# Performance work log

Measured on AMD Instinct MI355X. Metric: run time of the kernel, lower is better.

## Reference

```python
import jax, jax.numpy as jnp
import numpy as np
import math

B, N, D, H, F = 2, 2048, 512, 8, 2048
DH = D // H
LN_EPS = 1e-5
PHASE_ALPHA = 0.1


def _layernorm(x, g, b):
    mu = jnp.mean(x, axis=-1, keepdims=True)
    var = jnp.mean(jnp.square(x - mu), axis=-1, keepdims=True)
    return (x - mu) * jax.lax.rsqrt(var + LN_EPS) * g + b


def setup_inputs() -> dict:
    key = jax.random.key(0)
    ks = jax.random.split(key, 16)
    s = 0.02
    return {
        "h": jax.random.normal(ks[0], (B, N, D), dtype=jnp.float32),
        "phases": jax.random.normal(ks[1], (B, N, H), dtype=jnp.float32),
        "mask": jnp.zeros((B, N), dtype=bool),
        "Wq": jax.random.normal(ks[2], (D, D), dtype=jnp.float32) * s,
        "Wk": jax.random.normal(ks[3], (D, D), dtype=jnp.float32) * s,
        "Wp": jax.random.normal(ks[4], (D, H), dtype=jnp.float32) * s,
        "bp": jnp.zeros((H,), dtype=jnp.float32),
        "Wv": jax.random.normal(ks[5], (D, D), dtype=jnp.float32) * s,
        "Wo": jax.random.normal(ks[6], (D, D), dtype=jnp.float32) * s,
        "W1": jax.random.normal(ks[7], (D, F), dtype=jnp.float32) * s,
        "b1": jnp.zeros((F,), dtype=jnp.float32),
        "W2": jax.random.normal(ks[8], (F, D), dtype=jnp.float32) * s,
        "b2": jnp.zeros((D,), dtype=jnp.float32),
        "g1": jnp.ones((D,), dtype=jnp.float32),
        "be1": jnp.zeros((D,), dtype=jnp.float32),
        "g2": jnp.ones((D,), dtype=jnp.float32),
        "be2": jnp.zeros((D,), dtype=jnp.float32),
        "Wph": jax.random.normal(ks[9], (D, H), dtype=jnp.float32) * s,
        "bph": jnp.zeros((H,), dtype=jnp.float32),
    }


def reference(h, phases, mask, Wq, Wk, Wp, bp, Wv, Wo, W1, b1, W2, b2, g1, be1, g2, be2, Wph, bph):
    # --- HarmonicEdgeLayer ---
    Q = (h @ Wq).reshape(B, N, H, DH)  # (B,N,H,dh)
    K = (h @ Wk).reshape(B, N, H, DH)
    scores = jnp.einsum("bnhd,bmhd->bhnm", Q, K) / math.sqrt(DH)  # (B,H,N,N)
    ph = h @ Wp + bp                       # (B,N,H)
    phi = jnp.transpose(ph, (0, 2, 1))     # (B,H,N)
    harmonic = jnp.cos(phi[:, :, :, None] - phi[:, :, None, :])  # (B,H,N,N)
    scores = scores * (1.0 + harmonic) * 0.5
    scores = jnp.where(mask[:, None, None, :], -jnp.inf, scores)
    edge_weights = jax.nn.softmax(scores, axis=-1)  # (B,H,N,N)

    # --- HarmonicNodeUpdate ---
    V = (h @ Wv).reshape(B, N, H, DH)
    messages = jnp.einsum("bhnm,bmhd->bnhd", edge_weights, V).reshape(B, N, D)
    messages = messages @ Wo
    h1 = _layernorm(h + messages, g1, be1)
    ffn = jax.nn.gelu(h1 @ W1 + b1, approximate=False) @ W2 + b2
    h2 = _layernorm(h1 + ffn, g2, be2)

    # --- PhaseUpdate ---
    phases_new = phases + PHASE_ALPHA * jnp.tanh(h2 @ Wph + bph) * math.pi

    # convergence metric
    delta = jnp.mean(jnp.linalg.norm(h2 - h, axis=-1))
    return h2, phases_new, delta
```

## Files before the change

### kernel.cpp

```cpp
#include <hip/hip_runtime.h>
#include <math.h>

#define BB 2
#define NN 2048
#define DD 512
#define HH 8
#define DHH 64
#define FF 2048
#define MROWS (BB*NN)
#define LN_EPS 1e-5f
#define PHASE_ALPHA 0.1f
#define PI_F 3.14159265358979323846f
#define SCALE 0.125f
#define QLD (3*DD)

typedef __attribute__((ext_vector_type(8))) short  bf16x8;
typedef __attribute__((ext_vector_type(4))) float  f32x4;
typedef __attribute__((ext_vector_type(4))) unsigned short us4;

__device__ __forceinline__ unsigned short f2bf(float x) {
    unsigned int u = __float_as_uint(x);
    u += 0x7fffu + ((u >> 16) & 1u);
    return (unsigned short)(u >> 16);
}

__global__ __launch_bounds__(256) void convert_bf16_kernel(
    const float* __restrict__ X, unsigned short* __restrict__ Y, int n8)
{
    int i = blockIdx.x*256 + threadIdx.x;
    if (i >= n8) return;
    const float4 a = *(const float4*)&X[i*8];
    const float4 b = *(const float4*)&X[i*8 + 4];
    uint4 o;
    o.x = (unsigned)f2bf(a.x) | ((unsigned)f2bf(a.y) << 16);
    o.y = (unsigned)f2bf(a.z) | ((unsigned)f2bf(a.w) << 16);
    o.z = (unsigned)f2bf(b.x) | ((unsigned)f2bf(b.y) << 16);
    o.w = (unsigned)f2bf(b.z) | ((unsigned)f2bf(b.w) << 16);
    *(uint4*)&Y[i*8] = o;
}

__global__ __launch_bounds__(256) void wtrans_kernel(
    const float* __restrict__ W, unsigned short* __restrict__ WT, int K, int N)
{
    __shared__ unsigned short T[32][33];
    const int k0 = blockIdx.y*32, n0 = blockIdx.x*32;
    const int r = threadIdx.x >> 3, cc = (threadIdx.x & 7)*4;
    float4 v = *(const float4*)&W[(size_t)(k0 + r)*N + n0 + cc];
    T[cc+0][r] = f2bf(v.x); T[cc+1][r] = f2bf(v.y);
    T[cc+2][r] = f2bf(v.z); T[cc+3][r] = f2bf(v.w);
    __syncthreads();
    us4 o; o.x = T[r][cc]; o.y = T[r][cc+1]; o.z = T[r][cc+2]; o.w = T[r][cc+3];
    *(us4*)&WT[(size_t)(n0 + r)*K + k0 + cc] = o;
}

__global__ __launch_bounds__(256) void vtrans_kernel(
    const unsigned short* __restrict__ qkv, unsigned short* __restrict__ VT)
{
    __shared__ unsigned short T[32][33];
    const int b = blockIdx.z;
    const int n0 = blockIdx.x*32, c0 = blockIdx.y*32;
    const int r = threadIdx.x >> 3, cc = (threadIdx.x & 7)*4;
    us4 v = *(const us4*)&qkv[((size_t)b*NN + n0 + r)*QLD + 2*DD + c0 + cc];
    T[cc+0][r] = v.x; T[cc+1][r] = v.y; T[cc+2][r] = v.z; T[cc+3][r] = v.w;
    __syncthreads();
    const int cg = c0 + r;
    const int hh = cg >> 6, dh = cg & 63;
    us4 o; o.x = T[r][cc]; o.y = T[r][cc+1]; o.z = T[r][cc+2]; o.w = T[r][cc+3];
    *(us4*)&VT[(((size_t)b*HH + hh)*DHH + dh)*NN + n0 + cc] = o;
}

template<int BM, int BN, int SPLITK, int OUTBF16, int BIAS, int ACT, int ATOMIC>
__global__ __launch_bounds__(256, 2) void mfma_gemm(
    const unsigned short* __restrict__ A, const unsigned short* __restrict__ BT,
    const float* __restrict__ bias, void* __restrict__ Cout,
    int M, int Nc, int K)
{
    constexpr int FM = BM/32, FN = BN/32;
    constexpr int ROWS = BM + BN;
    constexpr int NLOAD = ROWS*8/256;
    __shared__ unsigned short Ss[ROWS][72];

    const int tid = threadIdx.x;
    const int w = tid >> 6, lane = tid & 63;
    const int c = lane & 15, g = lane >> 4;
    const int wr = w >> 1, wc = w & 1;
    const int bm = blockIdx.y*BM, bn = blockIdx.x*BN;
    const int k0 = (SPLITK > 1) ? blockIdx.z * (K / SPLITK) : 0;
    const int NT = (K / SPLITK) / 64;

    f32x4 zero = {0.f, 0.f, 0.f, 0.f};
    f32x4 acc[FM][FN];
    #pragma unroll
    for (int i = 0; i < FM; ++i)
        #pragma unroll
        for (int j = 0; j < FN; ++j) acc[i][j] = zero;

    uint4 pf[NLOAD];
    #pragma unroll
    for (int l = 0; l < NLOAD; ++l) {
        const int i = tid + l*256;
        const int r = i >> 3, kc = (i & 7)*8;
        const unsigned short* src = (r < BM) ? &A [(size_t)(bm + r)*K + k0 + kc]
                                             : &BT[(size_t)(bn + r - BM)*K + k0 + kc];
        pf[l] = *(const uint4*)src;
    }

    for (int kt = 0; kt < NT; ++kt) {
        __syncthreads();
        #pragma unroll
        for (int l = 0; l < NLOAD; ++l) {
            const int i = tid + l*256;
            *(uint4*)&Ss[i >> 3][(i & 7)*8] = pf[l];
        }
        __syncthreads();
        if (kt + 1 < NT) {
            #pragma unroll
            for (int l = 0; l < NLOAD; ++l) {
                const int i = tid + l*256;
                const int r = i >> 3, kc = (i & 7)*8;
                const unsigned short* src = (r < BM)
                    ? &A [(size_t)(bm + r)*K + k0 + (kt+1)*64 + kc]
                    : &BT[(size_t)(bn + r - BM)*K + k0 + (kt+1)*64 + kc];
                pf[l] = *(const uint4*)src;
            }
        }
        #pragma unroll
        for (int ks = 0; ks < 2; ++ks) {
            bf16x8 af[FM], bfr[FN];
            #pragma unroll
            for (int mf = 0; mf < FM; ++mf)
                af[mf] = *(const bf16x8*)&Ss[wr*(BM/2) + mf*16 + c][ks*32 + g*8];
            #pragma unroll
            for (int nf = 0; nf < FN; ++nf)
                bfr[nf] = *(const bf16x8*)&Ss[BM + wc*(BN/2) + nf*16 + c][ks*32 + g*8];
            #pragma unroll
            for (int mf = 0; mf < FM; ++mf)
                #pragma unroll
                for (int nf = 0; nf < FN; ++nf)
                    acc[mf][nf] = __builtin_amdgcn_mfma_f32_16x16x32_bf16(
                        af[mf], bfr[nf], acc[mf][nf], 0, 0, 0);
        }
    }

    #pragma unroll
    for (int mf = 0; mf < FM; ++mf)
        #pragma unroll
        for (int nf = 0; nf < FN; ++nf) {
            const int col = bn + wc*(BN/2) + nf*16 + c;
            const float bv = BIAS ? bias[col] : 0.f;
            #pragma unroll
            for (int r = 0; r < 4; ++r) {
                const int row = bm + wr*(BM/2) + mf*16 + g*4 + r;
                float x = acc[mf][nf][r] + bv;
                if (ACT == 1) x = 0.5f * x * (1.f + erff(x * 0.70710678118654752f));
                if (ATOMIC)       atomicAdd(&((float*)Cout)[(size_t)row*Nc + col], x);
                else if (OUTBF16) ((unsigned short*)Cout)[(size_t)row*Nc + col] = f2bf(x);
                else              ((float*)Cout)[(size_t)row*Nc + col] = x;
            }
        }
}

__global__ __launch_bounds__(256) void phase_proj_kernel(
    const float* __restrict__ X, const float* __restrict__ Wp,
    const float* __restrict__ bp, float* __restrict__ cosPt, float* __restrict__ sinPt)
{
    __shared__ float Wl[DD*HH];
    for (int i = threadIdx.x; i < DD*HH; i += 256) Wl[i] = Wp[i];
    __syncthreads();
    int row = blockIdx.x*32 + (threadIdx.x >> 3);
    int hh  = threadIdx.x & 7;
    const float* xr = X + (size_t)row * DD;
    float acc = bp[hh];
    for (int k = 0; k < DD; k += 4) {
        float4 xv = *(const float4*)&xr[k];
        acc += xv.x*Wl[(k  )*HH+hh] + xv.y*Wl[(k+1)*HH+hh]
             + xv.z*Wl[(k+2)*HH+hh] + xv.w*Wl[(k+3)*HH+hh];
    }
    const int b = row >> 11, n = row & (NN-1);
    cosPt[((size_t)b*HH + hh)*NN + n] = cosf(acc);
    sinPt[((size_t)b*HH + hh)*NN + n] = sinf(acc);
}

__global__ __launch_bounds__(256) void phase_update_kernel(
    const float* __restrict__ H2, const float* __restrict__ Wph,
    const float* __restrict__ bph, const float* __restrict__ phases,
    float* __restrict__ phases_out)
{
    __shared__ float Wl[DD*HH];
    for (int i = threadIdx.x; i < DD*HH; i += 256) Wl[i] = Wph[i];
    __syncthreads();
    int row = blockIdx.x*32 + (threadIdx.x >> 3);
    int hh  = threadIdx.x & 7;
    const float* xr = H2 + (size_t)row * DD;
    float acc = bph[hh];
    for (int k = 0; k < DD; k += 4) {
        float4 xv = *(const float4*)&xr[k];
        acc += xv.x*Wl[(k  )*HH+hh] + xv.y*Wl[(k+1)*HH+hh]
             + xv.z*Wl[(k+2)*HH+hh] + xv.w*Wl[(k+3)*HH+hh];
    }
    phases_out[row*HH + hh] = phases[row*HH + hh] + PHASE_ALPHA * tanhf(acc) * PI_F;
}

__global__ __launch_bounds__(256, 2) void attn_kernel(
    const unsigned short* __restrict__ qkv, const unsigned short* __restrict__ VT,
    const float* __restrict__ cosPt, const float* __restrict__ sinPt,
    const unsigned char* __restrict__ mask, unsigned short* __restrict__ msgb)
{
    __shared__ float Os[64][68];
    __shared__ float MwS[4][64], LwS[4][64];
    __shared__ unsigned short Pl[4][64][40];

    const int tid = threadIdx.x;
    const int w = tid >> 6, lane = tid & 63;
    const int c = lane & 15, g = lane >> 4;
    const int qBase = blockIdx.x * 64;
    const int hh = blockIdx.y, b = blockIdx.z;
    const size_t rowOff = (size_t)b * NN;
    const int bh = b*HH + hh;
    const size_t cosBase = (size_t)bh * NN;

    for (int i = tid; i < 64*68; i += 256) ((float*)Os)[i] = 0.f;

    bf16x8 qf[4][2];
    #pragma unroll
    for (int nf = 0; nf < 4; ++nf)
        #pragma unroll
        for (int ks = 0; ks < 2; ++ks)
            qf[nf][ks] = *(const bf16x8*)&qkv[(rowOff + qBase + nf*16 + c)*QLD
                                              + hh*DHH + ks*32 + g*8];
    float cq[4], sq[4];
    #pragma unroll
    for (int nf = 0; nf < 4; ++nf) {
        cq[nf] = cosPt[cosBase + qBase + nf*16 + c];
        sq[nf] = sinPt[cosBase + qBase + nf*16 + c];
    }

    f32x4 zero = {0.f, 0.f, 0.f, 0.f};
    f32x4 acc[4][4];
    #pragma unroll
    for (int i = 0; i < 4; ++i)
        #pragma unroll
        for (int j = 0; j < 4; ++j) acc[i][j] = zero;
    float mst[4], lst[4];
    #pragma unroll
    for (int i = 0; i < 4; ++i) { mst[i] = -INFINITY; lst[i] = 0.f; }

    __syncthreads();

    for (int s = w; s < NN/32; s += 4) {
        const int kb0 = s * 32;
        f32x4 st[2][4];
        #pragma unroll
        for (int mf = 0; mf < 2; ++mf) {
            bf16x8 kf0 = *(const bf16x8*)&qkv[(rowOff + kb0 + mf*16 + c)*QLD + DD + hh*DHH + g*8];
            bf16x8 kf1 = *(const bf16x8*)&qkv[(rowOff + kb0 + mf*16 + c)*QLD + DD + hh*DHH + 32 + g*8];
            #pragma unroll
            for (int nf = 0; nf < 4; ++nf) {
                st[mf][nf] = __builtin_amdgcn_mfma_f32_16x16x32_bf16(kf0, qf[nf][0], zero, 0, 0, 0);
                st[mf][nf] = __builtin_amdgcn_mfma_f32_16x16x32_bf16(kf1, qf[nf][1], st[mf][nf], 0, 0, 0);
            }
        }
        #pragma unroll
        for (int mf = 0; mf < 2; ++mf) {
            const int keyb = kb0 + mf*16 + g*4;
            const f32x4 ck = *(const f32x4*)&cosPt[cosBase + keyb];
            const f32x4 sk = *(const f32x4*)&sinPt[cosBase + keyb];
            const unsigned int mk = *(const unsigned int*)&mask[rowOff + keyb];
            #pragma unroll
            for (int nf = 0; nf < 4; ++nf)
                #pragma unroll
                for (int r = 0; r < 4; ++r) {
                    float wgt = 0.5f + 0.5f*(cq[nf]*ck[r] + sq[nf]*sk[r]);
                    float v = st[mf][nf][r] * SCALE * wgt;
                    st[mf][nf][r] = ((mk >> (8*r)) & 0xff) ? -INFINITY : v;
                }
        }
        #pragma unroll
        for (int nf = 0; nf < 4; ++nf) {
            float tmax = -INFINITY;
            #pragma unroll
            for (int mf = 0; mf < 2; ++mf)
                #pragma unroll
                for (int r = 0; r < 4; ++r) tmax = fmaxf(tmax, st[mf][nf][r]);
            tmax = fmaxf(tmax, __shfl_xor(tmax, 16));
            tmax = fmaxf(tmax, __shfl_xor(tmax, 32));
            const float mnew = fmaxf(mst[nf], tmax);
            const float corr = (mst[nf] == -INFINITY) ? 0.f : __expf(mst[nf] - mnew);
            float psum = 0.f;
            unsigned short* prow = &Pl[w][nf*16 + c][0];
            #pragma unroll
            for (int mf = 0; mf < 2; ++mf) {
                float p0 = __expf(st[mf][nf][0] - mnew);
                float p1 = __expf(st[mf][nf][1] - mnew);
                float p2 = __expf(st[mf][nf][2] - mnew);
                float p3 = __expf(st[mf][nf][3] - mnew);
                psum += (p0 + p1) + (p2 + p3);
                *(unsigned int*)&prow[mf*16 + g*4    ] = (unsigned)f2bf(p0) | ((unsigned)f2bf(p1) << 16);
                *(unsigned int*)&prow[mf*16 + g*4 + 2] = (unsigned)f2bf(p2) | ((unsigned)f2bf(p3) << 16);
            }
            psum += __shfl_xor(psum, 16);
            psum += __shfl_xor(psum, 32);
            lst[nf] = lst[nf]*corr + psum;
            mst[nf] = mnew;
            #pragma unroll
            for (int mo = 0; mo < 4; ++mo)
                #pragma unroll
                for (int r = 0; r < 4; ++r) acc[mo][nf][r] *= corr;
        }
        bf16x8 vf[4], pfr[4];
        #pragma unroll
        for (int mo = 0; mo < 4; ++mo)
            vf[mo] = *(const bf16x8*)&VT[((size_t)bh*DHH + mo*16 + c)*NN + kb0 + g*8];
        #pragma unroll
        for (int nf = 0; nf < 4; ++nf)
            pfr[nf] = *(const bf16x8*)&Pl[w][nf*16 + c][g*8];
        #pragma unroll
        for (int mo = 0; mo < 4; ++mo)
            #pragma unroll
            for (int nf = 0; nf < 4; ++nf)
                acc[mo][nf] = __builtin_amdgcn_mfma_f32_16x16x32_bf16(
                    vf[mo], pfr[nf], acc[mo][nf], 0, 0, 0);
    }

    if (lane < 16) {
        #pragma unroll
        for (int nf = 0; nf < 4; ++nf) {
            MwS[w][nf*16 + lane] = mst[nf];
            LwS[w][nf*16 + lane] = lst[nf];
        }
    }
    __syncthreads();
    float fac[4];
    #pragma unroll
    for (int nf = 0; nf < 4; ++nf) {
        const int q = nf*16 + c;
        float M = fmaxf(fmaxf(MwS[0][q], MwS[1][q]), fmaxf(MwS[2][q], MwS[3][q]));
        float L = LwS[0][q]*__expf(MwS[0][q]-M) + LwS[1][q]*__expf(MwS[1][q]-M)
                + LwS[2][q]*__expf(MwS[2][q]-M) + LwS[3][q]*__expf(MwS[3][q]-M);
        fac[nf] = __expf(mst[nf] - M) / L;
    }
    #pragma unroll
    for (int mo = 0; mo < 4; ++mo)
        #pragma unroll
        for (int nf = 0; nf < 4; ++nf)
            #pragma unroll
            for (int r = 0; r < 4; ++r)
                atomicAdd(&Os[mo*16 + g*4 + r][nf*16 + c], acc[mo][nf][r] * fac[nf]);
    __syncthreads();

    const int q = tid >> 2, dh0 = (tid & 3) * 16;
    unsigned int ov[8];
    #pragma unroll
    for (int i = 0; i < 8; ++i)
        ov[i] = (unsigned)f2bf(Os[dh0 + 2*i][q]) | ((unsigned)f2bf(Os[dh0 + 2*i + 1][q]) << 16);
    unsigned short* op = &msgb[(rowOff + qBase + q)*DD + hh*DHH + dh0];
    *(uint4*)&op[0] = *(uint4*)&ov[0];
    *(uint4*)&op[8] = *(uint4*)&ov[4];
}

template<int WITH_DELTA, int WBF16, int YBIAS>
__global__ __launch_bounds__(256) void ln_kernel(
    const float* __restrict__ x, const float* __restrict__ y,
    const float* __restrict__ g, const float* __restrict__ bvec,
    const float* __restrict__ ybias,
    float* __restrict__ out, unsigned short* __restrict__ outb,
    const float* __restrict__ href, float* __restrict__ deltaAcc)
{
    const int row = blockIdx.x;
    const int tid = threadIdx.x;
    const size_t base = (size_t)row * DD + tid*2;
    float2 xv = *(const float2*)(x + base);
    float2 yv = *(const float2*)(y + base);
    float v0 = xv.x + yv.x;
    float v1 = xv.y + yv.y;
    if (YBIAS) { v0 += ybias[tid*2]; v1 += ybias[tid*2+1]; }
    float s  = v0 + v1;
    float sq = v0*v0 + v1*v1;
    #pragma unroll
    for (int m = 1; m < 64; m <<= 1) {
        s  += __shfl_xor(s,  m, 64);
        sq += __shfl_xor(sq, m, 64);
    }
    __shared__ float redS[4], redQ[4];
    int wv = tid >> 6;
    if ((tid & 63) == 0) { redS[wv] = s; redQ[wv] = sq; }
    __syncthreads();
    s  = redS[0] + redS[1] + redS[2] + redS[3];
    sq = redQ[0] + redQ[1] + redQ[2] + redQ[3];
    float mu  = s * (1.f/DD);
    float var = sq * (1.f/DD) - mu*mu;
    float inv = rsqrtf(var + LN_EPS);
    float o0 = (v0 - mu)*inv*g[tid*2  ] + bvec[tid*2  ];
    float o1 = (v1 - mu)*inv*g[tid*2+1] + bvec[tid*2+1];
    float2 ov; ov.x = o0; ov.y = o1;
    *(float2*)(out + base) = ov;
    if (WBF16)
        ((unsigned int*)outb)[(size_t)row*(DD/2) + tid] =
            (unsigned)f2bf(o0) | ((unsigned)f2bf(o1) << 16);

    if (WITH_DELTA) {
        float d0 = o0 - href[base], d1 = o1 - href[base + 1];
        float ds = d0*d0 + d1*d1;
        #pragma unroll
        for (int m = 1; m < 64; m <<= 1) ds += __shfl_xor(ds, m, 64);
        __shared__ float redD[4];
        if ((tid & 63) == 0) redD[wv] = ds;
        __syncthreads();
        if (tid == 0) {
            float t = redD[0] + redD[1] + redD[2] + redD[3];
            atomicAdd(deltaAcc, sqrtf(t));
        }
    }
}

__global__ void delta_finalize(const float* __restrict__ acc, float* __restrict__ out)
{
    out[0] = acc[0] * (1.f / (float)MROWS);
}

extern "C" void kernel_launch(void* const* d_in, const int* in_sizes, int n_in,
                              void* d_out, int out_size, void* d_ws, size_t ws_size,
                              hipStream_t stream)
{
    (void)in_sizes; (void)n_in; (void)out_size; (void)ws_size;
    const float* h      = (const float*)d_in[0];
    const float* phases = (const float*)d_in[1];
    const unsigned char* mask = (const unsigned char*)d_in[2];
    const float* Wq  = (const float*)d_in[3];
    const float* Wk  = (const float*)d_in[4];
    const float* Wp  = (const float*)d_in[5];
    const float* bp  = (const float*)d_in[6];
    const float* Wv  = (const float*)d_in[7];
    const float* Wo  = (const float*)d_in[8];
    const float* W1  = (const float*)d_in[9];
    const float* b1  = (const float*)d_in[10];
    const float* W2  = (const float*)d_in[11];
    const float* b2  = (const float*)d_in[12];
    const float* g1  = (const float*)d_in[13];
    const float* be1 = (const float*)d_in[14];
    const float* g2  = (const float*)d_in[15];
    const float* be2 = (const float*)d_in[16];
    const float* Wph = (const float*)d_in[17];
    const float* bph = (const float*)d_in[18];

    char* ws = (char*)d_ws;
    const size_t MB = 1024*1024;
    unsigned short* hb   = (unsigned short*)(ws);
    unsigned short* WqT  = (unsigned short*)(ws + 4*MB);
    unsigned short* WkT  = (unsigned short*)(ws + 4*MB + 512*1024);
    unsigned short* WvT  = (unsigned short*)(ws + 5*MB);
    unsigned short* WoT  = (unsigned short*)(ws + 5*MB + 512*1024);
    unsigned short* W1T  = (unsigned short*)(ws + 6*MB);
    unsigned short* W2T  = (unsigned short*)(ws + 8*MB);
    unsigned short* qkvb = (unsigned short*)(ws + 10*MB);
    unsigned short* VT   = (unsigned short*)(ws + 22*MB);
    unsigned short* T1b  = qkvb;
    unsigned short* msgb = (unsigned short*)(ws + 26*MB);
    float* mo    = (float*)(ws + 30*MB);
    float* ffn   = mo;
    float* h1    = (float*)(ws + 38*MB);
    unsigned short* h1b = (unsigned short*)(ws + 46*MB);
    float* cosPt = (float*)(ws + 50*MB);
    float* sinPt = (float*)(ws + 50*MB + 64*1024);
    float* dAcc  = (float*)(ws + 50*MB + 128*1024);

    float* out_h2    = (float*)d_out;
    float* out_ph    = out_h2 + (size_t)MROWS*DD;
    float* out_delta = out_ph + MROWS*HH;

    hipMemsetAsync(dAcc, 0, sizeof(float), stream);

    dim3 blk(256);
    convert_bf16_kernel<<<dim3(MROWS*DD/8/256), blk, 0, stream>>>(h, hb, MROWS*DD/8);
    wtrans_kernel<<<dim3(DD/32, DD/32), blk, 0, stream>>>(Wq, WqT, DD, DD);
    wtrans_kernel<<<dim3(DD/32, DD/32), blk, 0, stream>>>(Wk, WkT, DD, DD);
    wtrans_kernel<<<dim3(DD/32, DD/32), blk, 0, stream>>>(Wv, WvT, DD, DD);
    wtrans_kernel<<<dim3(DD/32, DD/32), blk, 0, stream>>>(Wo, WoT, DD, DD);
    wtrans_kernel<<<dim3(FF/32, DD/32), blk, 0, stream>>>(W1, W1T, DD, FF);
    wtrans_kernel<<<dim3(DD/32, FF/32), blk, 0, stream>>>(W2, W2T, FF, DD);
    phase_proj_kernel<<<dim3(MROWS/32), blk, 0, stream>>>(h, Wp, bp, cosPt, sinPt);
    mfma_gemm<64,128,1,1,0,0,0><<<dim3((3*DD)/128, MROWS/64), blk, 0, stream>>>(
        hb, WqT, nullptr, qkvb, MROWS, 3*DD, DD);
    vtrans_kernel<<<dim3(NN/32, DD/32, BB), blk, 0, stream>>>(qkvb, VT);
    attn_kernel<<<dim3(NN/64, HH, BB), blk, 0, stream>>>(qkvb, VT, cosPt, sinPt, mask, msgb);
    mfma_gemm<64,64,1,0,0,0,0><<<dim3(DD/64, MROWS/64), blk, 0, stream>>>(
        msgb, WoT, nullptr, mo, MROWS, DD, DD);
    ln_kernel<0,1,0><<<dim3(MROWS), blk, 0, stream>>>(h, mo, g1, be1, nullptr, h1, h1b, nullptr, nullptr);
    mfma_gemm<128,128,1,1,1,1,0><<<dim3(FF/128, MROWS/128), blk, 0, stream>>>(
        h1b, W1T, b1, T1b, MROWS, FF, DD);
    hipMemsetAsync(ffn, 0, (size_t)MROWS*DD*sizeof(float), stream);
    mfma_gemm<64,64,2,0,0,0,1><<<dim3(DD/64, MROWS/64, 2), blk, 0, stream>>>(
        T1b, W2T, nullptr, ffn, MROWS, DD, FF);
    ln_kernel<1,0,1><<<dim3(MROWS), blk, 0, stream>>>(h1, ffn, g2, be2, b2, out_h2, nullptr, h, dAcc);
    phase_update_kernel<<<dim3(MROWS/32), blk, 0, stream>>>(out_h2, Wph, bph, phases, out_ph);
    delta_finalize<<<dim3(1), dim3(1), 0, stream>>>(dAcc, out_delta);
}
```

Baseline: 511.5 us.

## Halve attention query tile, use exp2 with folded scale, lazy rescale, packed bf16 convert

```diff
diff --git a/kernel.cpp b/kernel.cpp
--- a/kernel.cpp
+++ b/kernel.cpp
@@ -13,6 +13,7 @@
 #define PI_F 3.14159265358979323846f
 #define SCALE 0.125f
 #define QLD (3*DD)
+#define LOG2E 1.44269504088896340736f
 
 typedef __attribute__((ext_vector_type(8))) short  bf16x8;
 typedef __attribute__((ext_vector_type(4))) float  f32x4;
@@ -22,6 +23,18 @@
     unsigned int u = __float_as_uint(x);
     u += 0x7fffu + ((u >> 16) & 1u);
     return (unsigned short)(u >> 16);
+}
+
+#if __has_builtin(__builtin_amdgcn_exp2f)
+#define EXP2(x) __builtin_amdgcn_exp2f(x)
+#else
+#define EXP2(x) exp2f(x)
+#endif
+
+__device__ __forceinline__ unsigned pk_bf16(float a, float b) {
+    unsigned r;
+    asm("v_cvt_pk_bf16_f32 %0, %1, %2" : "=v"(r) : "v"(a), "v"(b));
+    return r;
 }
 
 __global__ __launch_bounds__(256) void convert_bf16_kernel(
@@ -201,61 +214,60 @@
     phases_out[row*HH + hh] = phases[row*HH + hh] + PHASE_ALPHA * tanhf(acc) * PI_F;
 }
 
-__global__ __launch_bounds__(256, 2) void attn_kernel(
+__global__ __launch_bounds__(256, 4) void attn_kernel(
     const unsigned short* __restrict__ qkv, const unsigned short* __restrict__ VT,
     const float* __restrict__ cosPt, const float* __restrict__ sinPt,
     const unsigned char* __restrict__ mask, unsigned short* __restrict__ msgb)
 {
-    __shared__ float Os[64][68];
-    __shared__ float MwS[4][64], LwS[4][64];
-    __shared__ unsigned short Pl[4][64][40];
+    __shared__ float Os[64][36];
+    __shared__ float MwS[4][32], LwS[4][32];
+    __shared__ unsigned short Pl[4][32][40];
 
     const int tid = threadIdx.x;
     const int w = tid >> 6, lane = tid & 63;
     const int c = lane & 15, g = lane >> 4;
-    const int qBase = blockIdx.x * 64;
+    const int qBase = blockIdx.x * 32;
     const int hh = blockIdx.y, b = blockIdx.z;
     const size_t rowOff = (size_t)b * NN;
     const int bh = b*HH + hh;
     const size_t cosBase = (size_t)bh * NN;
-
-    for (int i = tid; i < 64*68; i += 256) ((float*)Os)[i] = 0.f;
-
-    bf16x8 qf[4][2];
-    #pragma unroll
-    for (int nf = 0; nf < 4; ++nf)
+    const float A = 0.5f * SCALE * LOG2E;
+
+    for (int i = tid; i < 64*36; i += 256) ((float*)Os)[i] = 0.f;
+
+    bf16x8 qf[2][2];
+    #pragma unroll
+    for (int nf = 0; nf < 2; ++nf)
         #pragma unroll
         for (int ks = 0; ks < 2; ++ks)
             qf[nf][ks] = *(const bf16x8*)&qkv[(rowOff + qBase + nf*16 + c)*QLD
                                               + hh*DHH + ks*32 + g*8];
-    float cq[4], sq[4];
-    #pragma unroll
-    for (int nf = 0; nf < 4; ++nf) {
-        cq[nf] = cosPt[cosBase + qBase + nf*16 + c];
-        sq[nf] = sinPt[cosBase + qBase + nf*16 + c];
+    float cqs[2], sqs[2];
+    #pragma unroll
+    for (int nf = 0; nf < 2; ++nf) {
+        cqs[nf] = A * cosPt[cosBase + qBase + nf*16 + c];
+        sqs[nf] = A * sinPt[cosBase + qBase + nf*16 + c];
     }
 
     f32x4 zero = {0.f, 0.f, 0.f, 0.f};
-    f32x4 acc[4][4];
+    f32x4 acc[4][2];
     #pragma unroll
     for (int i = 0; i < 4; ++i)
         #pragma unroll
-        for (int j = 0; j < 4; ++j) acc[i][j] = zero;
-    float mst[4], lst[4];
-    #pragma unroll
-    for (int i = 0; i < 4; ++i) { mst[i] = -INFINITY; lst[i] = 0.f; }
+        for (int j = 0; j < 2; ++j) acc[i][j] = zero;
+    float mst[2] = {-INFINITY, -INFINITY}, lst[2] = {0.f, 0.f};
 
     __syncthreads();
 
     for (int s = w; s < NN/32; s += 4) {
         const int kb0 = s * 32;
-        f32x4 st[2][4];
+        f32x4 st[2][2];
         #pragma unroll
         for (int mf = 0; mf < 2; ++mf) {
             bf16x8 kf0 = *(const bf16x8*)&qkv[(rowOff + kb0 + mf*16 + c)*QLD + DD + hh*DHH + g*8];
             bf16x8 kf1 = *(const bf16x8*)&qkv[(rowOff + kb0 + mf*16 + c)*QLD + DD + hh*DHH + 32 + g*8];
             #pragma unroll
-            for (int nf = 0; nf < 4; ++nf) {
+            for (int nf = 0; nf < 2; ++nf) {
                 st[mf][nf] = __builtin_amdgcn_mfma_f32_16x16x32_bf16(kf0, qf[nf][0], zero, 0, 0, 0);
                 st[mf][nf] = __builtin_amdgcn_mfma_f32_16x16x32_bf16(kf1, qf[nf][1], st[mf][nf], 0, 0, 0);
             }
@@ -266,96 +278,99 @@
             const f32x4 ck = *(const f32x4*)&cosPt[cosBase + keyb];
             const f32x4 sk = *(const f32x4*)&sinPt[cosBase + keyb];
             const unsigned int mk = *(const unsigned int*)&mask[rowOff + keyb];
-            #pragma unroll
-            for (int nf = 0; nf < 4; ++nf)
+            f32x4 mbias;
+            #pragma unroll
+            for (int r = 0; r < 4; ++r)
+                mbias[r] = ((mk >> (8*r)) & 0xff) ? -INFINITY : 0.f;
+            #pragma unroll
+            for (int nf = 0; nf < 2; ++nf)
                 #pragma unroll
                 for (int r = 0; r < 4; ++r) {
-                    float wgt = 0.5f + 0.5f*(cq[nf]*ck[r] + sq[nf]*sk[r]);
-                    float v = st[mf][nf][r] * SCALE * wgt;
-                    st[mf][nf][r] = ((mk >> (8*r)) & 0xff) ? -INFINITY : v;
+                    const float factor = fmaf(cqs[nf], ck[r], fmaf(sqs[nf], sk[r], A));
+                    st[mf][nf][r] = fmaf(st[mf][nf][r], factor, mbias[r]);
                 }
         }
         #pragma unroll
-        for (int nf = 0; nf < 4; ++nf) {
-            float tmax = -INFINITY;
-            #pragma unroll
-            for (int mf = 0; mf < 2; ++mf)
-                #pragma unroll
-                for (int r = 0; r < 4; ++r) tmax = fmaxf(tmax, st[mf][nf][r]);
+        for (int nf = 0; nf < 2; ++nf) {
+            float tmax = fmaxf(fmaxf(st[0][nf][0], st[0][nf][1]), fmaxf(st[0][nf][2], st[0][nf][3]));
+            tmax = fmaxf(tmax, fmaxf(fmaxf(st[1][nf][0], st[1][nf][1]), fmaxf(st[1][nf][2], st[1][nf][3])));
             tmax = fmaxf(tmax, __shfl_xor(tmax, 16));
             tmax = fmaxf(tmax, __shfl_xor(tmax, 32));
-            const float mnew = fmaxf(mst[nf], tmax);
-            const float corr = (mst[nf] == -INFINITY) ? 0.f : __expf(mst[nf] - mnew);
+            if (!__all(tmax <= mst[nf])) {
+                const float mnew = fmaxf(mst[nf], tmax);
+                const float corr = (mst[nf] == -INFINITY) ? 0.f : EXP2(mst[nf] - mnew);
+                lst[nf] *= corr;
+                #pragma unroll
+                for (int mo = 0; mo < 4; ++mo)
+                    #pragma unroll
+                    for (int r = 0; r < 4; ++r) acc[mo][nf][r] *= corr;
+                mst[nf] = mnew;
+            }
+            const float mcur = mst[nf];
             float psum = 0.f;
             unsigned short* prow = &Pl[w][nf*16 + c][0];
             #pragma unroll
             for (int mf = 0; mf < 2; ++mf) {
-                float p0 = __expf(st[mf][nf][0] - mnew);
-                float p1 = __expf(st[mf][nf][1] - mnew);
-                float p2 = __expf(st[mf][nf][2] - mnew);
-                float p3 = __expf(st[mf][nf][3] - mnew);
+                float p0 = EXP2(st[mf][nf][0] - mcur);
+                float p1 = EXP2(st[mf][nf][1] - mcur);
+                float p2 = EXP2(st[mf][nf][2] - mcur);
+                float p3 = EXP2(st[mf][nf][3] - mcur);
                 psum += (p0 + p1) + (p2 + p3);
-                *(unsigned int*)&prow[mf*16 + g*4    ] = (unsigned)f2bf(p0) | ((unsigned)f2bf(p1) << 16);
-                *(unsigned int*)&prow[mf*16 + g*4 + 2] = (unsigned)f2bf(p2) | ((unsigned)f2bf(p3) << 16);
+                uint2 pk; pk.x = pk_bf16(p0, p1); pk.y = pk_bf16(p2, p3);
+                *(uint2*)&prow[mf*16 + g*4] = pk;
             }
             psum += __shfl_xor(psum, 16);
             psum += __shfl_xor(psum, 32);
-            lst[nf] = lst[nf]*corr + psum;
-            mst[nf] = mnew;
-            #pragma unroll
-            for (int mo = 0; mo < 4; ++mo)
-                #pragma unroll
-                for (int r = 0; r < 4; ++r) acc[mo][nf][r] *= corr;
-        }
-        bf16x8 vf[4], pfr[4];
+            lst[nf] += psum;
+        }
+        bf16x8 vf[4], pfr[2];
         #pragma unroll
         for (int mo = 0; mo < 4; ++mo)
             vf[mo] = *(const bf16x8*)&VT[((size_t)bh*DHH + mo*16 + c)*NN + kb0 + g*8];
         #pragma unroll
-        for (int nf = 0; nf < 4; ++nf)
+        for (int nf = 0; nf < 2; ++nf)
             pfr[nf] = *(const bf16x8*)&Pl[w][nf*16 + c][g*8];
         #pragma unroll
         for (int mo = 0; mo < 4; ++mo)
             #pragma unroll
-            for (int nf = 0; nf < 4; ++nf)
+            for (int nf = 0; nf < 2; ++nf)
                 acc[mo][nf] = __builtin_amdgcn_mfma_f32_16x16x32_bf16(
                     vf[mo], pfr[nf], acc[mo][nf], 0, 0, 0);
     }
 
     if (lane < 16) {
         #pragma unroll
-        for (int nf = 0; nf < 4; ++nf) {
+        for (int nf = 0; nf < 2; ++nf) {
             MwS[w][nf*16 + lane] = mst[nf];
             LwS[w][nf*16 + lane] = lst[nf];
         }
     }
     __syncthreads();
-    float fac[4];
-    #pragma unroll
-    for (int nf = 0; nf < 4; ++nf) {
+    float fac[2];
+    #pragma unroll
+    for (int nf = 0; nf < 2; ++nf) {
         const int q = nf*16 + c;
         float M = fmaxf(fmaxf(MwS[0][q], MwS[1][q]), fmaxf(MwS[2][q], MwS[3][q]));
-        float L = LwS[0][q]*__expf(MwS[0][q]-M) + LwS[1][q]*__expf(MwS[1][q]-M)
-                + LwS[2][q]*__expf(MwS[2][q]-M) + LwS[3][q]*__expf(MwS[3][q]-M);
-        fac[nf] = __expf(mst[nf] - M) / L;
+        float L = LwS[0][q]*EXP2(MwS[0][q]-M) + LwS[1][q]*EXP2(MwS[1][q]-M)
+                + LwS[2][q]*EXP2(MwS[2][q]-M) + LwS[3][q]*EXP2(MwS[3][q]-M);
+        fac[nf] = EXP2(mst[nf] - M) / L;
     }
     #pragma unroll
     for (int mo = 0; mo < 4; ++mo)
         #pragma unroll
-        for (int nf = 0; nf < 4; ++nf)
+        for (int nf = 0; nf < 2; ++nf)
             #pragma unroll
             for (int r = 0; r < 4; ++r)
                 atomicAdd(&Os[mo*16 + g*4 + r][nf*16 + c], acc[mo][nf][r] * fac[nf]);
     __syncthreads();
 
-    const int q = tid >> 2, dh0 = (tid & 3) * 16;
-    unsigned int ov[8];
-    #pragma unroll
-    for (int i = 0; i < 8; ++i)
+    const int q = tid >> 3, dh0 = (tid & 7) * 8;
+    unsigned int ov[4];
+    #pragma unroll
+    for (int i = 0; i < 4; ++i)
         ov[i] = (unsigned)f2bf(Os[dh0 + 2*i][q]) | ((unsigned)f2bf(Os[dh0 + 2*i + 1][q]) << 16);
     unsigned short* op = &msgb[(rowOff + qBase + q)*DD + hh*DHH + dh0];
     *(uint4*)&op[0] = *(uint4*)&ov[0];
-    *(uint4*)&op[8] = *(uint4*)&ov[4];
 }
 
 template<int WITH_DELTA, int WBF16, int YBIAS>
@@ -482,7 +497,7 @@
     mfma_gemm<64,128,1,1,0,0,0><<<dim3((3*DD)/128, MROWS/64), blk, 0, stream>>>(
         hb, WqT, nullptr, qkvb, MROWS, 3*DD, DD);
     vtrans_kernel<<<dim3(NN/32, DD/32, BB), blk, 0, stream>>>(qkvb, VT);
-    attn_kernel<<<dim3(NN/64, HH, BB), blk, 0, stream>>>(qkvb, VT, cosPt, sinPt, mask, msgb);
+    attn_kernel<<<dim3(NN/32, HH, BB), blk, 0, stream>>>(qkvb, VT, cosPt, sinPt, mask, msgb);
     mfma_gemm<64,64,1,0,0,0,0><<<dim3(DD/64, MROWS/64), blk, 0, stream>>>(
         msgb, WoT, nullptr, mo, MROWS, DD, DD);
     ln_kernel<0,1,0><<<dim3(MROWS), blk, 0, stream>>>(h, mo, g1, be1, nullptr, h1, h1b, nullptr, nullptr);
```

After: 523.7 us. 2.4% more time.
